# Performance work log

Hardware: AMD Instinct MI355X
Metric: run time of the kernel (lower is better)

The kernel has to match this reference:

```python
import jax, jax.numpy as jnp
import numpy as np
from jax import lax

B, N, H, W, C = 8, 1024, 256, 256, 256
HID = 512
RATES = (1, 3, 9, 9, 3, 1)


def setup_inputs() -> dict:
    key = jax.random.key(0)
    ks = jax.random.split(key, 16)
    # vertices are (row, col) float coordinates inside the feature map
    vertices = jax.random.uniform(ks[0], (B, N, 2), jnp.float32) * jnp.array([H - 1, W - 1], jnp.float32)
    features = jax.random.normal(ks[1], (B, H, W, C), jnp.float32)
    inp = {"vertices": vertices, "features": features}
    # Conv1D stack params (haiku Conv1D: kernel [K, Cin, Cout], bias [Cout])
    cin = C
    for i in range(6):
        inp[f"w{i}"] = jax.random.normal(ks[2 + 2 * i], (3, cin, HID), jnp.float32) * 0.05
        inp[f"b{i}"] = jax.random.normal(ks[3 + 2 * i], (HID,), jnp.float32) * 0.05
        cin = HID
    # offset head: Conv1D(2, 1, with_bias=False); original zero-init, randomized here
    inp["w_off"] = jax.random.normal(ks[14], (1, HID, 2), jnp.float32) * 0.05
    return inp


def _conv1d(x, w, b, rate):
    # x: [B, N, Cin], w: [K, Cin, Cout] -> SAME-padded dilated conv over vertex axis
    y = lax.conv_general_dilated(x, w, window_strides=(1,), padding="SAME",
                                 rhs_dilation=(rate,),
                                 dimension_numbers=("NWC", "WIO", "NWC"))
    return y if b is None else y + b


def _sample_at_vertices(vertices, features):
    # bilinear interpolation, zero outside (map_coordinates order=1 mode='constant')
    Bb, Hh, Ww, Cc = features.shape
    y, x = vertices[..., 0], vertices[..., 1]  # [B, N]
    y0f, x0f = jnp.floor(y), jnp.floor(x)
    wy1, wx1 = y - y0f, x - x0f
    wy0, wx0 = 1.0 - wy1, 1.0 - wx1
    y0, x0 = y0f.astype(jnp.int32), x0f.astype(jnp.int32)
    flat = features.reshape(Bb, Hh * Ww, Cc)

    def gather(yi, xi, wgt):
        valid = (yi >= 0) & (yi < Hh) & (xi >= 0) & (xi < Ww)
        idx = jnp.clip(yi, 0, Hh - 1) * Ww + jnp.clip(xi, 0, Ww - 1)  # [B, N]
        vals = jnp.take_along_axis(flat, idx[..., None], axis=1)  # [B, N, C]
        return vals * (wgt * valid)[..., None]

    return (gather(y0, x0, wy0 * wx0) + gather(y0, x0 + 1, wy0 * wx1)
            + gather(y0 + 1, x0, wy1 * wx0) + gather(y0 + 1, x0 + 1, wy1 * wx1))


def reference(vertices, features, w0, b0, w1, b1, w2, b2, w3, b3, w4, b4, w5, b5, w_off):
    h = _sample_at_vertices(vertices, features)  # [B, N, C]
    ws = (w0, w1, w2, w3, w4, w5)
    bs = (b0, b1, b2, b3, b4, b5)
    for w, b, r in zip(ws, bs, RATES):
        h = jax.nn.relu(_conv1d(h, w, b, r))
    offsets = _conv1d(h, w_off, None, 1)  # [B, N, 2]
    return vertices + offsets
```

## Files before the change

kernel.cpp:

```cpp
#include <hip/hip_runtime.h>

#define BATCH 8
#define NPTS  1024
#define FH    256
#define FW    256
#define FC    256
#define HID   512
#define PADN  1056
#define HALO  16

typedef __attribute__((ext_vector_type(8))) short short8;
typedef __attribute__((ext_vector_type(16))) float f32x16;
typedef unsigned short ushort_t;
typedef unsigned int uint_t;

__device__ __forceinline__ ushort_t f2bf(float f) {
    uint_t u = __builtin_bit_cast(uint_t, f);
    u += 0x7fffu + ((u >> 16) & 1u);
    return (ushort_t)(u >> 16);
}
__device__ __forceinline__ float bf2f(ushort_t s) {
    uint_t u = ((uint_t)s) << 16;
    return __builtin_bit_cast(float, u);
}

#define GLOAD16(g, l)                                                     \
    __builtin_amdgcn_global_load_lds(                                     \
        (const __attribute__((address_space(1))) void*)(g),               \
        (__attribute__((address_space(3))) void*)(l), 16, 0, 0)

__device__ __forceinline__ short8 ldsread16(const short* p) {
    short8 r;
    const __attribute__((address_space(3))) short* p3 =
        (const __attribute__((address_space(3))) short*)p;
    asm volatile("ds_read_b128 %0, %1" : "=v"(r) : "v"(p3));
    return r;
}
__device__ __forceinline__ short8 gread16(const short* p) {
    short8 r;
    asm volatile("global_load_dwordx4 %0, %1, off" : "=v"(r) : "v"(p));
    return r;
}

__global__ __launch_bounds__(256) void prep_kernel(
    const float* __restrict__ vertices, const float* __restrict__ features,
    const float* __restrict__ w0, const float* __restrict__ w1,
    const float* __restrict__ w2, const float* __restrict__ w3,
    const float* __restrict__ w4, const float* __restrict__ w5,
    ushort_t* __restrict__ wt0, ushort_t* __restrict__ wt1,
    ushort_t* __restrict__ wt2, ushort_t* __restrict__ wt3,
    ushort_t* __restrict__ wt4, ushort_t* __restrict__ wt5,
    ushort_t* __restrict__ XpA, ushort_t* __restrict__ XpB,
    ushort_t* __restrict__ XpC)
{
    __shared__ float tile[64][65];
    const int blk = blockIdx.x;
    const int tid = threadIdx.x;

    if (blk < 1280) {
        int i = blk * 256 + tid;
        if (i < 65536) {
            int b = i >> 13, rem = i & 8191;
            int strip = rem >> 12, off = rem & 4095;
            XpA[(size_t)b * (PADN * FC) + (strip ? (PADN - HALO) * FC : 0) + off] = 0;
        }
        int jB = i - 65536;
        if (jB >= 0 && jB < 262144) {
            ushort_t* T = (jB < 131072) ? XpB : XpC;
            int j = jB & 131071;
            int b = j >> 14, rem = j & 16383;
            int strip = rem >> 13, off = rem & 8191;
            T[(size_t)b * (PADN * HID) + (strip ? (PADN - HALO) * HID : 0) + off] = 0;
        }
        return;
    }

    if (blk < 2336) {
        int j = blk - 1280;
        const float* w; ushort_t* wt; int CIN, kk0, co0;
        if (j < 96) {
            w = w0; wt = wt0; CIN = FC;
            kk0 = (j % 12) * 64; co0 = (j / 12) * 64;
        } else {
            int j2 = j - 96;
            int layer = j2 / 192, jj = j2 % 192;
            const float* ws[5]  = {w1, w2, w3, w4, w5};
            ushort_t*   wts[5]  = {wt1, wt2, wt3, wt4, wt5};
            w = ws[layer]; wt = wts[layer]; CIN = HID;
            kk0 = (jj % 24) * 64; co0 = (jj / 24) * 64;
        }
        int tap = kk0 / CIN, ci0 = kk0 - tap * CIN;
        int SL  = (3 * CIN) >> 4;
#pragma unroll 4
        for (int it = 0; it < 16; ++it) {
            int r = it * 4 + (tid >> 6);
            tile[r][tid & 63] = w[((size_t)tap * CIN + ci0 + r) * HID + co0 + (tid & 63)];
        }
        __syncthreads();
        int gl  = tid >> 7;
        int r2  = tid & 127;
        int l   = r2 >> 1;
        int j0  = (r2 & 1) * 4;
        int gco = (co0 >> 5) + gl;
        int kb  = ((l >> 5) << 3);
        int cl  = gl * 32 + (l & 31);
#pragma unroll
        for (int si = 0; si < 4; ++si) {
            int s = (kk0 >> 4) + si;
            ushort4 v;
            v.x = f2bf(tile[si * 16 + kb + j0 + 0][cl]);
            v.y = f2bf(tile[si * 16 + kb + j0 + 1][cl]);
            v.z = f2bf(tile[si * 16 + kb + j0 + 2][cl]);
            v.w = f2bf(tile[si * 16 + kb + j0 + 3][cl]);
            *(ushort4*)(wt + ((((size_t)gco * SL) + s) << 9) + l * 8 + j0) = v;
        }
        return;
    }

    {
        int p = (blk - 2336) * 4 + (tid >> 6);
        int b = p >> 10;
        int n = p & 1023;
        int t = tid & 63;

        float y = vertices[2 * p + 0];
        float x = vertices[2 * p + 1];
        float y0f = floorf(y), x0f = floorf(x);
        float wy1 = y - y0f, wx1 = x - x0f;
        float wy0 = 1.f - wy1, wx0 = 1.f - wx1;
        int y0 = (int)y0f, x0 = (int)x0f;

        float4 acc = make_float4(0.f, 0.f, 0.f, 0.f);
        const float4* fbase = (const float4*)features + (size_t)b * FH * FW * (FC / 4);

#define CORNER(yi, xi, wgt) {                                                  \
        int yy = (yi), xx = (xi);                                              \
        float wv = ((yy >= 0) && (yy < FH) && (xx >= 0) && (xx < FW)) ? (wgt) : 0.f; \
        int yc = yy < 0 ? 0 : (yy > FH - 1 ? FH - 1 : yy);                     \
        int xc = xx < 0 ? 0 : (xx > FW - 1 ? FW - 1 : xx);                     \
        float4 v = fbase[((size_t)yc * FW + xc) * (FC / 4) + t];               \
        acc.x += v.x * wv; acc.y += v.y * wv; acc.z += v.z * wv; acc.w += v.w * wv; }

        CORNER(y0,     x0,     wy0 * wx0);
        CORNER(y0,     x0 + 1, wy0 * wx1);
        CORNER(y0 + 1, x0,     wy1 * wx0);
        CORNER(y0 + 1, x0 + 1, wy1 * wx1);
#undef CORNER

        ushort4 o;
        o.x = f2bf(acc.x); o.y = f2bf(acc.y); o.z = f2bf(acc.z); o.w = f2bf(acc.w);
        *(ushort4*)(XpA + ((size_t)b * PADN + HALO + n) * FC + 4 * t) = o;
    }
}

template <int CIN>
__global__ __launch_bounds__(256) void conv_mfma(
    const ushort_t* __restrict__ Xp,
    const ushort_t* __restrict__ Wf,
    const float* __restrict__ bias,
    ushort_t* __restrict__ Yp,
    int rate)
{
    constexpr int K3 = 3 * CIN;
    constexpr int NT = K3 / 64;
    constexpr int SL = K3 / 16;
    __shared__ short lds[3][8192];

    const int tid  = threadIdx.x;
    const int wid  = tid >> 6;
    const int lane = tid & 63;
    const int wm   = wid >> 1, wn = wid & 1;

    const int h  = blockIdx.x;
    const int bm = (h & 7) * 8 + (h >> 6);
    const int bn = (h >> 3) & 7;
    const int batch = bm >> 3;
    const int n0    = (bm & 7) * 128;
    const int co0   = bn * 64;

    const short* Xbase = (const short*)Xp + ((size_t)batch * PADN + HALO + n0) * CIN;
    const short* Wb = (const short*)Wf
                    + (((size_t)(bn * 2 + wn) * SL) << 9) + lane * 8;

    auto stageA = [&](int buf, int kt) {
        const int tap = (kt << 6) / CIN;
        const int ci0 = (kt << 6) - tap * CIN;
        const short* Ag = Xbase + (ptrdiff_t)(tap - 1) * rate * CIN + ci0;
        short* ldsA = &lds[buf][0];
#pragma unroll
        for (int it = 0; it < 4; ++it) {
            int row  = wid * 32 + it * 8 + (lane >> 3);
            int chnk = (lane & 7) ^ (row & 7);
            GLOAD16(Ag + (size_t)row * CIN + chnk * 8, ldsA + ((wid * 4 + it) << 9));
        }
    };
    auto loadB = [&](short8* dst, int kt) {
        const short* p = Wb + ((size_t)(kt * 4) << 9);
#pragma unroll
        for (int ks = 0; ks < 4; ++ks) dst[ks] = gread16(p + (ks << 9));
    };

    f32x16 acc[2];
    const int rowA0 = wm * 64 + (lane & 31);
    const int coB   = wn * 32 + (lane & 31);
    {
        float bv = bias[co0 + coB];
#pragma unroll
        for (int i = 0; i < 2; ++i)
#pragma unroll
            for (int r = 0; r < 16; ++r) acc[i][r] = bv;
    }

    short8 B0[4], B1[4];
    stageA(0, 0);
    __builtin_amdgcn_sched_barrier(0);
    loadB(B0, 0);
    __builtin_amdgcn_sched_barrier(0);
    stageA(1, 1);
    __builtin_amdgcn_sched_barrier(0);

    int cur = 0;
    auto kstep = [&](int s, short8* Bcur, short8* Bnxt) {
        if (s == NT - 1) asm volatile("s_waitcnt vmcnt(0)" ::: "memory");
        else             asm volatile("s_waitcnt vmcnt(4)" ::: "memory");
        __builtin_amdgcn_s_barrier();
        __builtin_amdgcn_sched_barrier(0);

        if (s + 1 < NT) loadB(Bnxt, s + 1);
        __builtin_amdgcn_sched_barrier(0);
        if (s + 2 < NT) {
            int nb = cur + 2; if (nb >= 3) nb -= 3;
            stageA(nb, s + 2);
        }
        __builtin_amdgcn_sched_barrier(0);

        const short* As = &lds[cur][0];
        short8 av[2][4];
#pragma unroll
        for (int ks = 0; ks < 4; ++ks) {
            int ch = ks * 2 + (lane >> 5);
#pragma unroll
            for (int i = 0; i < 2; ++i) {
                int ra = rowA0 + i * 32;
                av[i][ks] = ldsread16(As + ra * 64 + ((ch ^ (ra & 7)) << 3));
            }
        }
        asm volatile("s_waitcnt lgkmcnt(0)" ::: "memory");
        __builtin_amdgcn_sched_barrier(0);
        __builtin_amdgcn_s_setprio(1);
#pragma unroll
        for (int ks = 0; ks < 4; ++ks)
#pragma unroll
            for (int i = 0; i < 2; ++i)
                acc[i] = __builtin_amdgcn_mfma_f32_32x32x16_bf16(
                    av[i][ks], Bcur[ks], acc[i], 0, 0, 0);
        __builtin_amdgcn_s_setprio(0);
        cur += 1; if (cur >= 3) cur -= 3;
    };

    for (int kt = 0; kt < NT; kt += 2) {
        kstep(kt,     B0, B1);
        kstep(kt + 1, B1, B0);
    }

    ushort_t* Yb = Yp + ((size_t)batch * PADN + HALO + n0) * HID + co0;
#pragma unroll
    for (int i = 0; i < 2; ++i) {
#pragma unroll
        for (int r = 0; r < 16; ++r) {
            int rrow = wm * 64 + i * 32 + (r & 3) + 8 * (r >> 2) + 4 * (lane >> 5);
            float v = acc[i][r];
            v = v > 0.f ? v : 0.f;
            Yb[(size_t)rrow * HID + coB] = f2bf(v);
        }
    }
}

__global__ __launch_bounds__(64) void head_kernel(
    const ushort_t* __restrict__ h, const float* __restrict__ w_off,
    const float* __restrict__ vertices, float* __restrict__ out)
{
    int p = blockIdx.x;
    int b = p >> 10, n = p & 1023;
    int t = threadIdx.x;
    const ushort_t* hr = h + ((size_t)b * PADN + HALO + n) * HID + t * 8;

    uint4 raw = *(const uint4*)hr;
    ushort_t hv[8];
    hv[0] = raw.x & 0xffff; hv[1] = raw.x >> 16;
    hv[2] = raw.y & 0xffff; hv[3] = raw.y >> 16;
    hv[4] = raw.z & 0xffff; hv[5] = raw.z >> 16;
    hv[6] = raw.w & 0xffff; hv[7] = raw.w >> 16;

    float s0 = 0.f, s1 = 0.f;
#pragma unroll
    for (int k = 0; k < 8; ++k) {
        float x = bf2f(hv[k]);
        s0 += x * w_off[(t * 8 + k) * 2 + 0];
        s1 += x * w_off[(t * 8 + k) * 2 + 1];
    }
#pragma unroll
    for (int off = 32; off >= 1; off >>= 1) {
        s0 += __shfl_down(s0, off);
        s1 += __shfl_down(s1, off);
    }
    if (t == 0) {
        out[2 * p + 0] = vertices[2 * p + 0] + s0;
        out[2 * p + 1] = vertices[2 * p + 1] + s1;
    }
}

extern "C" void kernel_launch(void* const* d_in, const int* in_sizes, int n_in,
                              void* d_out, int out_size, void* d_ws, size_t ws_size,
                              hipStream_t stream)
{
    (void)in_sizes; (void)n_in; (void)out_size; (void)ws_size;

    const float* vertices = (const float*)d_in[0];
    const float* features = (const float*)d_in[1];
    const float* w[6]  = {(const float*)d_in[2], (const float*)d_in[4],
                          (const float*)d_in[6], (const float*)d_in[8],
                          (const float*)d_in[10], (const float*)d_in[12]};
    const float* bb[6] = {(const float*)d_in[3], (const float*)d_in[5],
                          (const float*)d_in[7], (const float*)d_in[9],
                          (const float*)d_in[11], (const float*)d_in[13]};
    const float* w_off = (const float*)d_in[14];
    float* out = (float*)d_out;

    char* p = (char*)d_ws;
    ushort_t* wt[6];
    wt[0] = (ushort_t*)p; p += (size_t)HID * (3 * FC) * 2;
    for (int i = 1; i < 6; ++i) { wt[i] = (ushort_t*)p; p += (size_t)HID * (3 * HID) * 2; }
    ushort_t* XpA = (ushort_t*)p; p += (size_t)BATCH * PADN * FC  * 2;
    ushort_t* XpB = (ushort_t*)p; p += (size_t)BATCH * PADN * HID * 2;
    ushort_t* XpC = (ushort_t*)p;

    prep_kernel<<<4384, 256, 0, stream>>>(
        vertices, features, w[0], w[1], w[2], w[3], w[4], w[5],
        wt[0], wt[1], wt[2], wt[3], wt[4], wt[5], XpA, XpB, XpC);

    static const int rates[6] = {1, 3, 9, 9, 3, 1};
    conv_mfma<FC><<<512, 256, 0, stream>>>(XpA, wt[0], bb[0], XpB, rates[0]);
    ushort_t* src = XpB;
    ushort_t* dst = XpC;
    for (int i = 1; i < 6; ++i) {
        conv_mfma<HID><<<512, 256, 0, stream>>>(src, wt[i], bb[i], dst, rates[i]);
        ushort_t* tmp = src; src = dst; dst = tmp;
    }

    head_kernel<<<BATCH * NPTS, 64, 0, stream>>>(src, w_off, vertices, out);
}
```

Measured before the change: 137.1 us.

## Stage haloed input tile once per channel chunk and reuse across all three taps

The conv kernel now loads a 160-row haloed activation tile per 64-channel chunk into LDS and reads all three dilated taps from it at row offsets, instead of staging a separate 128-row tile for each tap. This cuts global-to-LDS traffic for the A operand roughly threefold, but triples the B-register buffers to 12 per stage and enlarges LDS per block. Launch bounds now request 2 blocks per SM, and the explicit inline-asm LDS reads are replaced with plain loads the compiler can schedule. The register and LDS growth may reduce occupancy. The tile also relies on the halo covering the maximum dilation of 9, which a 16-row halo does.

```diff
diff --git a/kernel.cpp b/kernel.cpp
--- a/kernel.cpp
+++ b/kernel.cpp
@@ -29,13 +29,6 @@
         (const __attribute__((address_space(1))) void*)(g),               \
         (__attribute__((address_space(3))) void*)(l), 16, 0, 0)
 
-__device__ __forceinline__ short8 ldsread16(const short* p) {
-    short8 r;
-    const __attribute__((address_space(3))) short* p3 =
-        (const __attribute__((address_space(3))) short*)p;
-    asm volatile("ds_read_b128 %0, %1" : "=v"(r) : "v"(p3));
-    return r;
-}
 __device__ __forceinline__ short8 gread16(const short* p) {
     short8 r;
     asm volatile("global_load_dwordx4 %0, %1, off" : "=v"(r) : "v"(p));
@@ -154,17 +147,17 @@
 }
 
 template <int CIN>
-__global__ __launch_bounds__(256) void conv_mfma(
+__global__ __launch_bounds__(256, 2) void conv_mfma(
     const ushort_t* __restrict__ Xp,
     const ushort_t* __restrict__ Wf,
     const float* __restrict__ bias,
     ushort_t* __restrict__ Yp,
     int rate)
 {
-    constexpr int K3 = 3 * CIN;
-    constexpr int NT = K3 / 64;
-    constexpr int SL = K3 / 16;
-    __shared__ short lds[3][8192];
+    constexpr int NC  = CIN / 64;
+    constexpr int SL3 = CIN / 16;
+    constexpr int SL  = 3 * SL3;
+    __shared__ short lds[3][10240];
 
     const int tid  = threadIdx.x;
     const int wid  = tid >> 6;
@@ -178,26 +171,28 @@
     const int n0    = (bm & 7) * 128;
     const int co0   = bn * 64;
 
-    const short* Xbase = (const short*)Xp + ((size_t)batch * PADN + HALO + n0) * CIN;
+    const short* Xbase = (const short*)Xp + ((size_t)batch * PADN + n0) * CIN;
     const short* Wb = (const short*)Wf
                     + (((size_t)(bn * 2 + wn) * SL) << 9) + lane * 8;
 
-    auto stageA = [&](int buf, int kt) {
-        const int tap = (kt << 6) / CIN;
-        const int ci0 = (kt << 6) - tap * CIN;
-        const short* Ag = Xbase + (ptrdiff_t)(tap - 1) * rate * CIN + ci0;
+    auto stageA = [&](int buf, int c) {
+        const short* Ag = Xbase + c * 64;
         short* ldsA = &lds[buf][0];
 #pragma unroll
-        for (int it = 0; it < 4; ++it) {
-            int row  = wid * 32 + it * 8 + (lane >> 3);
-            int chnk = (lane & 7) ^ (row & 7);
-            GLOAD16(Ag + (size_t)row * CIN + chnk * 8, ldsA + ((wid * 4 + it) << 9));
+        for (int it = 0; it < 5; ++it) {
+            int slot = it * 256 + wid * 64 + lane;
+            int row  = slot >> 3;
+            int chnk = (slot & 7) ^ (row & 7);
+            GLOAD16(Ag + (size_t)row * CIN + chnk * 8,
+                    ldsA + (size_t)(it * 256 + wid * 64) * 8);
         }
     };
-    auto loadB = [&](short8* dst, int kt) {
-        const short* p = Wb + ((size_t)(kt * 4) << 9);
-#pragma unroll
-        for (int ks = 0; ks < 4; ++ks) dst[ks] = gread16(p + (ks << 9));
+    auto loadB = [&](short8* dst, int c) {
+#pragma unroll
+        for (int t = 0; t < 3; ++t)
+#pragma unroll
+            for (int ks = 0; ks < 4; ++ks)
+                dst[t * 4 + ks] = gread16(Wb + ((size_t)(t * SL3 + c * 4 + ks) << 9));
     };
 
     f32x16 acc[2];
@@ -211,7 +206,7 @@
             for (int r = 0; r < 16; ++r) acc[i][r] = bv;
     }
 
-    short8 B0[4], B1[4];
+    short8 B0[12], B1[12];
     stageA(0, 0);
     __builtin_amdgcn_sched_barrier(0);
     loadB(B0, 0);
@@ -220,47 +215,49 @@
     __builtin_amdgcn_sched_barrier(0);
 
     int cur = 0;
-    auto kstep = [&](int s, short8* Bcur, short8* Bnxt) {
-        if (s == NT - 1) asm volatile("s_waitcnt vmcnt(0)" ::: "memory");
-        else             asm volatile("s_waitcnt vmcnt(4)" ::: "memory");
+    auto kstep = [&](int c, short8* Bcur, short8* Bnxt) {
+        if (c == NC - 1) asm volatile("s_waitcnt vmcnt(0)" ::: "memory");
+        else             asm volatile("s_waitcnt vmcnt(5)" ::: "memory");
         __builtin_amdgcn_s_barrier();
         __builtin_amdgcn_sched_barrier(0);
 
-        if (s + 1 < NT) loadB(Bnxt, s + 1);
+        if (c + 1 < NC) loadB(Bnxt, c + 1);
         __builtin_amdgcn_sched_barrier(0);
-        if (s + 2 < NT) {
+        if (c + 2 < NC) {
             int nb = cur + 2; if (nb >= 3) nb -= 3;
-            stageA(nb, s + 2);
+            stageA(nb, c + 2);
         }
         __builtin_amdgcn_sched_barrier(0);
 
         const short* As = &lds[cur][0];
-        short8 av[2][4];
-#pragma unroll
-        for (int ks = 0; ks < 4; ++ks) {
-            int ch = ks * 2 + (lane >> 5);
-#pragma unroll
-            for (int i = 0; i < 2; ++i) {
-                int ra = rowA0 + i * 32;
-                av[i][ks] = ldsread16(As + ra * 64 + ((ch ^ (ra & 7)) << 3));
+        __builtin_amdgcn_s_setprio(1);
+#pragma unroll
+        for (int t = 0; t < 3; ++t) {
+            const int shift = 16 + (t - 1) * rate;
+            short8 av[2][4];
+#pragma unroll
+            for (int ks = 0; ks < 4; ++ks) {
+                int ch = ks * 2 + (lane >> 5);
+#pragma unroll
+                for (int i = 0; i < 2; ++i) {
+                    int rr = rowA0 + i * 32 + shift;
+                    av[i][ks] = *(const short8*)(As + rr * 64 + ((ch ^ (rr & 7)) << 3));
+                }
             }
-        }
-        asm volatile("s_waitcnt lgkmcnt(0)" ::: "memory");
-        __builtin_amdgcn_sched_barrier(0);
-        __builtin_amdgcn_s_setprio(1);
-#pragma unroll
-        for (int ks = 0; ks < 4; ++ks)
-#pragma unroll
-            for (int i = 0; i < 2; ++i)
-                acc[i] = __builtin_amdgcn_mfma_f32_32x32x16_bf16(
-                    av[i][ks], Bcur[ks], acc[i], 0, 0, 0);
+#pragma unroll
+            for (int ks = 0; ks < 4; ++ks)
+#pragma unroll
+                for (int i = 0; i < 2; ++i)
+                    acc[i] = __builtin_amdgcn_mfma_f32_32x32x16_bf16(
+                        av[i][ks], Bcur[t * 4 + ks], acc[i], 0, 0, 0);
+        }
         __builtin_amdgcn_s_setprio(0);
         cur += 1; if (cur >= 3) cur -= 3;
     };
 
-    for (int kt = 0; kt < NT; kt += 2) {
-        kstep(kt,     B0, B1);
-        kstep(kt + 1, B1, B0);
+    for (int c = 0; c < NC; c += 2) {
+        kstep(c,     B0, B1);
+        kstep(c + 1, B1, B0);
     }
 
     ushort_t* Yb = Yp + ((size_t)batch * PADN + HALO + n0) * HID + co0;
```

New measurement: 121.9 us. -11.1%, faster.
